# Kernel tuning notes

Measured on AMD Instinct MI355X. Metric: run time of the kernel, lower is better.

The kernel has to match this reference:

```python
import jax, jax.numpy as jnp
import numpy as np
from jax import lax

K_NEIGHBORS = 128  # args.k_neighbors


def setup_inputs() -> dict:
    key = jax.random.key(0)
    k1, k2, k3 = jax.random.split(key, 3)
    images = jax.random.normal(k1, (16, 3, 32, 32), dtype=jnp.float32)
    # patch dictionary: [n_patches=2048, C_in=3, p=6, p=6]
    kernel = jax.random.normal(k2, (2048, 3, 6, 6), dtype=jnp.float32)
    # bias = squared patch norms / 2 (positive), shape [n_patches]
    bias = jax.random.uniform(k3, (2048,), dtype=jnp.float32)
    return {"images": images, "kernel": kernel, "bias": bias}


def _conv(images, kernel):
    # NCHW x OIHW -> NCHW, VALID conv (matches F.conv2d with no padding/stride)
    return lax.conv_general_dilated(
        images, kernel, window_strides=(1, 1), padding='VALID',
        dimension_numbers=('NCHW', 'OIHW', 'NCHW'))


def reference(images, kernel, bias):
    conv = _conv(images, kernel)                       # [B, P, H', W']
    # hflip of kernel = flip along last (width) axis
    conv_flip = _conv(images, kernel[..., ::-1])       # [B, P, H', W']
    b = bias[None, :, None, None]                      # [1, P, 1, 1]
    # order matches torch: [pos, flipped_pos, neg, flipped_neg]
    d = jnp.concatenate([-conv + b, -conv_flip + b, conv + b, conv_flip + b],
                        axis=1)                        # [B, 4P, H', W']
    # torch kthvalue(k=K+1, dim=1) -> (K+1)-th smallest = 0-indexed K after partition
    kth = jnp.partition(d, K_NEIGHBORS, axis=1)[:, K_NEIGHBORS:K_NEIGHBORS + 1]
    return jnp.where(d < kth, jnp.float32(1.0), jnp.float32(0.0))
```

## Files before the change

kernel.cpp:

```cpp
#include <hip/hip_runtime.h>


#define NPOS 729
#define NTHR 11664
#define FCH 16

__device__ __forceinline__ unsigned map32(float x) {
    unsigned v = __float_as_uint(x);
    return (v & 0x80000000u) ? ~v : (v | 0x80000000u);
}

__global__ __launch_bounds__(128) void prep_w1(
    const float* __restrict__ wgt, float* __restrict__ s1)
{
    int f = blockIdx.x;
    int t = threadIdx.x;
    s1[f * 128 + t] = (t < 108) ? wgt[f * 108 + t] : 0.f;
}

#define RLW(pos) __int_as_float(__builtin_amdgcn_readlane(                      \
    ((pos) < 64 ? wv0 : wv1), (pos) & 63))
#define WIDX(ci, kh, kw) (((ci) * 6 + (kh)) * 6 + (kw))

__global__ __launch_bounds__(256) void conv_rl34(
    const float* __restrict__ img, const float* __restrict__ s1,
    float4* __restrict__ Bp)
{
    int bx = blockIdx.x;
    int fg = bx & 127;
    int rest = bx >> 7;
    int pg = rest % 3;
    int n  = rest / 3;
    int t  = threadIdx.x;
    int lane = t & 63;

    bool act = t < 243;
    int p  = pg * 243 + (act ? t : 242);
    int oh = p / 27, ow = p % 27;

    float x[3][6][6];
    #pragma unroll
    for (int ci = 0; ci < 3; ci++)
        #pragma unroll
        for (int kh = 0; kh < 6; kh++)
            #pragma unroll
            for (int kw = 0; kw < 6; kw++)
                x[ci][kh][kw] = img[((n * 3 + ci) * 32 + oh + kh) * 32 + ow + kw];

    const int* sw = (const int*)s1;
    int f0 = fg * FCH;
    int wv0 = sw[f0 * 128 + lane];
    int wv1 = sw[f0 * 128 + 64 + lane];

    #pragma unroll 1
    for (int fi = 0; fi < FCH; fi++) {
        int f = f0 + fi;
        int nf = (fi == FCH - 1) ? f : (f + 1);
        int nv0 = sw[nf * 128 + lane];
        int nv1 = sw[nf * 128 + 64 + lane];

        float c3 = 0.f, cf3 = 0.f, c4 = 0.f, cf4 = 0.f;

        #pragma unroll
        for (int kh = 0; kh < 6; kh++)
            #pragma unroll
            for (int kw = 0; kw < 6; kw++)
                #pragma unroll
                for (int ci = 0; ci < 3; ci++) {
                    float wa = RLW(WIDX(ci, kh, kw));
                    float wb = RLW(WIDX(ci, kh, 5 - kw));
                    float xx = x[ci][kh][kw];
                    c3  = __fadd_rn(c3,  __fmul_rn(wa, xx));
                    cf3 = __fadd_rn(cf3, __fmul_rn(wb, xx));
                }

        #pragma unroll
        for (int kw = 0; kw < 6; kw++)
            #pragma unroll
            for (int kh = 0; kh < 6; kh++)
                #pragma unroll
                for (int ci = 0; ci < 3; ci++) {
                    float wa = RLW(WIDX(ci, kh, kw));
                    float wb = RLW(WIDX(ci, kh, 5 - kw));
                    float xx = x[ci][kh][kw];
                    c4  = fmaf(wa, xx, c4);
                    cf4 = fmaf(wb, xx, cf4);
                }

        if (act)
            Bp[((long)n * 2048 + f) * NPOS + p] = make_float4(c3, cf3, c4, cf4);
        wv0 = nv0; wv1 = nv1;
    }
}

__global__ __launch_bounds__(256) void thresh_kernel(
    const float4* __restrict__ Bp, const float* __restrict__ bias,
    unsigned* __restrict__ thr)
{
    int bx = blockIdx.x;
    int w  = (bx & 7) * 1458 + (bx >> 3);
    int n = w / NPOS;
    int p = w % NPOS;
    int t = threadIdx.x;
    int lane = t & 63, wid = t >> 6;

    unsigned m3[2][8], m4[2][8];
    #pragma unroll
    for (int j = 0; j < 8; j++) {
        int f = t + 256 * j;
        float4 v = Bp[((long)n * 2048 + f) * NPOS + p];
        float b = bias[f];
        m3[0][j] = min(map32(__fsub_rn(b, v.x)), map32(__fadd_rn(v.x, b)));
        m3[1][j] = min(map32(__fsub_rn(b, v.y)), map32(__fadd_rn(v.y, b)));
        m4[0][j] = min(map32(__fsub_rn(b, v.z)), map32(__fadd_rn(v.z, b)));
        m4[1][j] = min(map32(__fsub_rn(b, v.w)), map32(__fadd_rn(v.w, b)));
    }

    __shared__ int partial[2][4];
    unsigned P3 = 0, P4 = 0;
    #pragma unroll 1
    for (int bit = 31; bit >= 0; bit--) {
        unsigned C3 = P3 | (1u << bit);
        unsigned C4 = P4 | (1u << bit);
        int cnt = 0;
        #pragma unroll
        for (int k = 0; k < 2; k++)
        #pragma unroll
        for (int j = 0; j < 8; j++) {
            cnt += (m3[k][j] < C3) ? 1 : 0;
            cnt += (m4[k][j] < C4) ? (1 << 16) : 0;
        }
        #pragma unroll
        for (int off = 32; off >= 1; off >>= 1) cnt += __shfl_xor(cnt, off, 64);
        int par = bit & 1;
        if (lane == 0) partial[par][wid] = cnt;
        __syncthreads();
        int tot = partial[par][0] + partial[par][1] + partial[par][2] + partial[par][3];
        if ((tot & 0xFFFF) <= 128) P3 = C3;
        if ((tot >> 16)    <= 128) P4 = C4;
    }
    if (t == 0) {
        thr[n * NPOS + p]        = P3;
        thr[NTHR + n * NPOS + p] = P4;
    }
}

__global__ __launch_bounds__(256) void writeout(
    const float4* __restrict__ Bp, const float* __restrict__ bias,
    const unsigned* __restrict__ thr, float* __restrict__ out)
{
    int bx = blockIdx.x;
    int grp = bx % 3;
    int rest = bx / 3;
    int ftile = rest & 31;
    int n = rest >> 5;
    int t = threadIdx.x;
    int w = t >> 6, lane = t & 63;
    int p = (grp * 4 + w) * 64 + lane;
    bool act = p < NPOS;

    unsigned P3 = 0, P4 = 0;
    if (act) {
        P3 = thr[n * NPOS + p];
        P4 = thr[NTHR + n * NPOS + p];
    }
    long nb = (long)n * 8192 * NPOS;

    #pragma unroll 1
    for (int fi = 0; fi < 64; fi++) {
        int f = ftile * 64 + fi;
        float b = bias[f];
        if (act) {
            float4 v = Bp[((long)n * 2048 + f) * NPOS + p];
            int s0 = (map32(__fsub_rn(b, v.x)) < P3) && (map32(__fsub_rn(b, v.z)) < P4);
            int s1 = (map32(__fsub_rn(b, v.y)) < P3) && (map32(__fsub_rn(b, v.w)) < P4);
            int s2 = (map32(__fadd_rn(v.x, b)) < P3) && (map32(__fadd_rn(v.z, b)) < P4);
            int s3 = (map32(__fadd_rn(v.y, b)) < P3) && (map32(__fadd_rn(v.w, b)) < P4);
            out[nb + (long)(f       ) * NPOS + p] = s0 ? 1.0f : 0.0f;
            out[nb + (long)(f + 2048) * NPOS + p] = s1 ? 1.0f : 0.0f;
            out[nb + (long)(f + 4096) * NPOS + p] = s2 ? 1.0f : 0.0f;
            out[nb + (long)(f + 6144) * NPOS + p] = s3 ? 1.0f : 0.0f;
        }
    }
}

__global__ __launch_bounds__(256) void conv_h34(
    const float* __restrict__ img, const float* __restrict__ wgt,
    float* __restrict__ out)
{
    int bx = blockIdx.x;
    int ftile = bx & 31;
    int rest  = bx >> 5;
    int oh = rest % 27;
    int n  = rest / 27;
    int t  = threadIdx.x;

    __shared__ float wl[64][109];
    __shared__ float patch[3][6][32];
    for (int idx = t; idx < 64 * 108; idx += 256) {
        int fi = idx / 108, k = idx - fi * 108;
        wl[fi][k] = wgt[(ftile * 64 + fi) * 108 + k];
    }
    for (int idx = t; idx < 576; idx += 256) {
        int w = idx & 31, rr = idx >> 5;
        int ci = rr / 6, r = rr - ci * 6;
        patch[ci][r][w] = img[((n * 3 + ci) * 32 + (oh + r)) * 32 + w];
    }
    __syncthreads();

    int fidx = t & 63;
    int g    = t >> 6;
    int ow0  = g * 7;
    int ncols = (g < 3) ? 7 : 6;
    int f = ftile * 64 + fidx;
    long nb = (long)n * 8192 * NPOS;
    long pb = (long)oh * 27;

    #pragma unroll 1
    for (int i = 0; i < ncols; i++) {
        int ow = ow0 + i;
        float c3 = 0, cf3 = 0, c4 = 0, cf4 = 0;
        #pragma unroll
        for (int kh = 0; kh < 6; kh++)
        #pragma unroll
        for (int kw = 0; kw < 6; kw++)
        #pragma unroll
        for (int ci = 0; ci < 3; ci++) {
            float x = patch[ci][kh][ow + kw];
            c3  = __fadd_rn(c3,  __fmul_rn(wl[fidx][(ci*6+kh)*6 + kw],     x));
            cf3 = __fadd_rn(cf3, __fmul_rn(wl[fidx][(ci*6+kh)*6 + 5 - kw], x));
        }
        #pragma unroll
        for (int kw = 0; kw < 6; kw++)
        #pragma unroll
        for (int kh = 0; kh < 6; kh++)
        #pragma unroll
        for (int ci = 0; ci < 3; ci++) {
            float x = patch[ci][kh][ow + kw];
            c4  = fmaf(wl[fidx][(ci*6+kh)*6 + kw],     x, c4);
            cf4 = fmaf(wl[fidx][(ci*6+kh)*6 + 5 - kw], x, cf4);
        }
        long pp = pb + ow;
        out[nb + (long)(f       ) * NPOS + pp] = c3;
        out[nb + (long)(f + 2048) * NPOS + pp] = cf3;
        out[nb + (long)(f + 4096) * NPOS + pp] = c4;
        out[nb + (long)(f + 6144) * NPOS + pp] = cf4;
    }
}

__device__ __forceinline__ unsigned bisect128(const unsigned (&u)[4][8],
                                              int lane, int wid, int* partial)
{
    unsigned P = 0;
    #pragma unroll 1
    for (int bit = 31; bit >= 0; bit--) {
        unsigned C = P | (1u << bit);
        int cnt = 0;
        #pragma unroll
        for (int q = 0; q < 4; q++)
            #pragma unroll
            for (int j = 0; j < 8; j++) cnt += (u[q][j] < C) ? 1 : 0;
        #pragma unroll
        for (int off = 32; off >= 1; off >>= 1) cnt += __shfl_xor(cnt, off, 64);
        if (lane == 0) partial[wid] = cnt;
        __syncthreads();
        int tot = partial[0] + partial[1] + partial[2] + partial[3];
        __syncthreads();
        if (tot <= 128) P = C;
    }
    return P;
}

__global__ __launch_bounds__(256) void sel_h34(
    const float* __restrict__ bias, float* out)
{
    int bx = blockIdx.x;
    int n = bx / NPOS;
    int p = bx % NPOS;
    int t = threadIdx.x;
    int lane = t & 63, wid = t >> 6;
    __shared__ int partial[4];

    unsigned u3[4][8], u4[4][8];
    long nb = (long)n * 8192 * NPOS;
    #pragma unroll
    for (int j = 0; j < 8; j++) {
        int f = t + 256 * j;
        float c3  = out[nb + (long)(f       ) * NPOS + p];
        float cf3 = out[nb + (long)(f + 2048) * NPOS + p];
        float c4  = out[nb + (long)(f + 4096) * NPOS + p];
        float cf4 = out[nb + (long)(f + 6144) * NPOS + p];
        float b   = bias[f];
        u3[0][j] = map32(__fsub_rn(b, c3));
        u3[1][j] = map32(__fsub_rn(b, cf3));
        u3[2][j] = map32(__fadd_rn(c3, b));
        u3[3][j] = map32(__fadd_rn(cf3, b));
        u4[0][j] = map32(__fsub_rn(b, c4));
        u4[1][j] = map32(__fsub_rn(b, cf4));
        u4[2][j] = map32(__fadd_rn(c4, b));
        u4[3][j] = map32(__fadd_rn(cf4, b));
    }
    unsigned P3 = bisect128(u3, lane, wid, partial);
    unsigned P4 = bisect128(u4, lane, wid, partial);
    #pragma unroll
    for (int j = 0; j < 8; j++) {
        int f = t + 256 * j;
        #pragma unroll
        for (int q = 0; q < 4; q++) {
            int s = (u3[q][j] < P3) && (u4[q][j] < P4);
            out[nb + (long)(q * 2048 + f) * NPOS + p] = s ? 1.0f : 0.0f;
        }
    }
}

extern "C" void kernel_launch(void* const* d_in, const int* in_sizes, int n_in,
                              void* d_out, int out_size, void* d_ws, size_t ws_size,
                              hipStream_t stream)
{
    const float* img  = (const float*)d_in[0];
    const float* wgt  = (const float*)d_in[1];
    const float* bias = (const float*)d_in[2];
    float* out = (float*)d_out;

    size_t bpB  = (size_t)16 * 2048 * NPOS * sizeof(float4);
    size_t thrB = (size_t)2 * NTHR * sizeof(unsigned);
    size_t s1B  = (size_t)2048 * 128 * sizeof(float);
    size_t need = bpB + thrB + s1B;

    if (ws_size >= need) {
        float4*   Bp  = (float4*)d_ws;
        unsigned* thr = (unsigned*)((char*)d_ws + bpB);
        float*    s1  = (float*)((char*)d_ws + bpB + thrB);
        prep_w1<<<2048, 128, 0, stream>>>(wgt, s1);
        conv_rl34<<<128 * 3 * 16, 256, 0, stream>>>(img, s1, Bp);
        thresh_kernel<<<NTHR, 256, 0, stream>>>(Bp, bias, thr);
        writeout<<<16 * 32 * 3, 256, 0, stream>>>(Bp, bias, thr, out);
    } else {
        conv_h34<<<16 * 27 * 32, 256, 0, stream>>>(img, wgt, out);
        sel_h34<<<NTHR, 256, 0, stream>>>(bias, out);
    }
}
```

Before: 819.5 us.

## Fuse mask computation into threshold kernel and pass selections as ballot bitmasks

The threshold kernel now keeps each (n,p) column's values in registers after the radix search. It computes the four selection predicates there, packs them per wave with ballot, and writes the 64-bit masks back into the first half of that column's own workspace slots. The writeout kernel becomes a simple expander that reads four bitmask words per thread and writes the float outputs. This removes the second full pass over the large float4 intermediate buffer and the separate threshold array. The cost is extra register pressure in the selection kernel and scattered 8-byte mask writes.

```diff
diff --git a/kernel.cpp b/kernel.cpp
--- a/kernel.cpp
+++ b/kernel.cpp
@@ -93,9 +93,8 @@
     }
 }
 
-__global__ __launch_bounds__(256) void thresh_kernel(
-    const float4* __restrict__ Bp, const float* __restrict__ bias,
-    unsigned* __restrict__ thr)
+__global__ __launch_bounds__(256) void sel_fused(
+    float4* __restrict__ Bp, const float* __restrict__ bias)
 {
     int bx = blockIdx.x;
     int w  = (bx & 7) * 1458 + (bx >> 3);
@@ -104,16 +103,19 @@
     int t = threadIdx.x;
     int lane = t & 63, wid = t >> 6;
 
+    float4 v[8];
+    float  bb[8];
     unsigned m3[2][8], m4[2][8];
     #pragma unroll
     for (int j = 0; j < 8; j++) {
         int f = t + 256 * j;
-        float4 v = Bp[((long)n * 2048 + f) * NPOS + p];
-        float b = bias[f];
-        m3[0][j] = min(map32(__fsub_rn(b, v.x)), map32(__fadd_rn(v.x, b)));
-        m3[1][j] = min(map32(__fsub_rn(b, v.y)), map32(__fadd_rn(v.y, b)));
-        m4[0][j] = min(map32(__fsub_rn(b, v.z)), map32(__fadd_rn(v.z, b)));
-        m4[1][j] = min(map32(__fsub_rn(b, v.w)), map32(__fadd_rn(v.w, b)));
+        v[j]  = Bp[((long)n * 2048 + f) * NPOS + p];
+        bb[j] = bias[f];
+        float b = bb[j];
+        m3[0][j] = min(map32(__fsub_rn(b, v[j].x)), map32(__fadd_rn(v[j].x, b)));
+        m3[1][j] = min(map32(__fsub_rn(b, v[j].y)), map32(__fadd_rn(v[j].y, b)));
+        m4[0][j] = min(map32(__fsub_rn(b, v[j].z)), map32(__fadd_rn(v[j].z, b)));
+        m4[1][j] = min(map32(__fsub_rn(b, v[j].w)), map32(__fadd_rn(v[j].w, b)));
     }
 
     __shared__ int partial[2][4];
@@ -139,15 +141,32 @@
         if ((tot & 0xFFFF) <= 128) P3 = C3;
         if ((tot >> 16)    <= 128) P4 = C4;
     }
-    if (t == 0) {
-        thr[n * NPOS + p]        = P3;
-        thr[NTHR + n * NPOS + p] = P4;
-    }
-}
-
-__global__ __launch_bounds__(256) void writeout(
-    const float4* __restrict__ Bp, const float* __restrict__ bias,
-    const unsigned* __restrict__ thr, float* __restrict__ out)
+
+    unsigned long long* bw = (unsigned long long*)Bp;
+    long cb = ((long)n * 2048) * NPOS + p;
+    #pragma unroll
+    for (int j = 0; j < 8; j++) {
+        float b = bb[j];
+        int s0 = (map32(__fsub_rn(b, v[j].x)) < P3) && (map32(__fsub_rn(b, v[j].z)) < P4);
+        int s1 = (map32(__fsub_rn(b, v[j].y)) < P3) && (map32(__fsub_rn(b, v[j].w)) < P4);
+        int s2 = (map32(__fadd_rn(v[j].x, b)) < P3) && (map32(__fadd_rn(v[j].z, b)) < P4);
+        int s3 = (map32(__fadd_rn(v[j].y, b)) < P3) && (map32(__fadd_rn(v[j].w, b)) < P4);
+        unsigned long long w0 = __ballot(s0);
+        unsigned long long w1 = __ballot(s1);
+        unsigned long long w2 = __ballot(s2);
+        unsigned long long w3 = __ballot(s3);
+        if (lane == 0) {
+            int wbase = 4 * j + wid;
+            bw[(cb + (long)(wbase      ) * NPOS) * 2] = w0;
+            bw[(cb + (long)(wbase + 32 ) * NPOS) * 2] = w1;
+            bw[(cb + (long)(wbase + 64 ) * NPOS) * 2] = w2;
+            bw[(cb + (long)(wbase + 96 ) * NPOS) * 2] = w3;
+        }
+    }
+}
+
+__global__ __launch_bounds__(256) void expand(
+    const float4* __restrict__ Bp, float* __restrict__ out)
 {
     int bx = blockIdx.x;
     int grp = bx % 3;
@@ -158,28 +177,24 @@
     int w = t >> 6, lane = t & 63;
     int p = (grp * 4 + w) * 64 + lane;
     bool act = p < NPOS;
-
-    unsigned P3 = 0, P4 = 0;
-    if (act) {
-        P3 = thr[n * NPOS + p];
-        P4 = thr[NTHR + n * NPOS + p];
-    }
+    int pc = act ? p : (NPOS - 1);
+
+    const unsigned long long* bw = (const unsigned long long*)Bp;
+    long cb = ((long)n * 2048) * NPOS + pc;
+    unsigned long long w0 = bw[(cb + (long)(ftile      ) * NPOS) * 2];
+    unsigned long long w1 = bw[(cb + (long)(ftile + 32 ) * NPOS) * 2];
+    unsigned long long w2 = bw[(cb + (long)(ftile + 64 ) * NPOS) * 2];
+    unsigned long long w3 = bw[(cb + (long)(ftile + 96 ) * NPOS) * 2];
+
     long nb = (long)n * 8192 * NPOS;
-
     #pragma unroll 1
     for (int fi = 0; fi < 64; fi++) {
         int f = ftile * 64 + fi;
-        float b = bias[f];
         if (act) {
-            float4 v = Bp[((long)n * 2048 + f) * NPOS + p];
-            int s0 = (map32(__fsub_rn(b, v.x)) < P3) && (map32(__fsub_rn(b, v.z)) < P4);
-            int s1 = (map32(__fsub_rn(b, v.y)) < P3) && (map32(__fsub_rn(b, v.w)) < P4);
-            int s2 = (map32(__fadd_rn(v.x, b)) < P3) && (map32(__fadd_rn(v.z, b)) < P4);
-            int s3 = (map32(__fadd_rn(v.y, b)) < P3) && (map32(__fadd_rn(v.w, b)) < P4);
-            out[nb + (long)(f       ) * NPOS + p] = s0 ? 1.0f : 0.0f;
-            out[nb + (long)(f + 2048) * NPOS + p] = s1 ? 1.0f : 0.0f;
-            out[nb + (long)(f + 4096) * NPOS + p] = s2 ? 1.0f : 0.0f;
-            out[nb + (long)(f + 6144) * NPOS + p] = s3 ? 1.0f : 0.0f;
+            out[nb + (long)(f       ) * NPOS + p] = ((w0 >> fi) & 1) ? 1.0f : 0.0f;
+            out[nb + (long)(f + 2048) * NPOS + p] = ((w1 >> fi) & 1) ? 1.0f : 0.0f;
+            out[nb + (long)(f + 4096) * NPOS + p] = ((w2 >> fi) & 1) ? 1.0f : 0.0f;
+            out[nb + (long)(f + 6144) * NPOS + p] = ((w3 >> fi) & 1) ? 1.0f : 0.0f;
         }
     }
 }
@@ -323,18 +338,16 @@
     float* out = (float*)d_out;
 
     size_t bpB  = (size_t)16 * 2048 * NPOS * sizeof(float4);
-    size_t thrB = (size_t)2 * NTHR * sizeof(unsigned);
     size_t s1B  = (size_t)2048 * 128 * sizeof(float);
-    size_t need = bpB + thrB + s1B;
+    size_t need = bpB + s1B;
 
     if (ws_size >= need) {
-        float4*   Bp  = (float4*)d_ws;
-        unsigned* thr = (unsigned*)((char*)d_ws + bpB);
-        float*    s1  = (float*)((char*)d_ws + bpB + thrB);
+        float4* Bp = (float4*)d_ws;
+        float*  s1 = (float*)((char*)d_ws + bpB);
         prep_w1<<<2048, 128, 0, stream>>>(wgt, s1);
         conv_rl34<<<128 * 3 * 16, 256, 0, stream>>>(img, s1, Bp);
-        thresh_kernel<<<NTHR, 256, 0, stream>>>(Bp, bias, thr);
-        writeout<<<16 * 32 * 3, 256, 0, stream>>>(Bp, bias, thr, out);
+        sel_fused<<<NTHR, 256, 0, stream>>>(Bp, bias);
+        expand<<<16 * 32 * 3, 256, 0, stream>>>(Bp, out);
     } else {
         conv_h34<<<16 * 27 * 32, 256, 0, stream>>>(img, wgt, out);
         sel_h34<<<NTHR, 256, 0, stream>>>(bias, out);
```

Result: slower. 870.0 us (+6.2%).
